# Optimization experiments

Measured on AMD Instinct MI355X. Metric: run time of the kernel, lower is better.

## Reference

```python
import jax, jax.numpy as jnp
import numpy as np

NUM_USER = 60000
NUM_ITEM = 40000
DIM = 64
E_U, E_I, E_G = 720000, 480000, 1200000


def _spmm(vals, src, dst, emb, n_rows):
    # sparse.mm(A, emb): out[dst] += A[dst, src] * emb[src]
    return jax.ops.segment_sum(vals[:, None] * emb[src], dst, num_segments=n_rows)


def setup_inputs() -> dict:
    key = jax.random.key(0)
    ks = jax.random.split(key, 11)
    return {
        "users_emb": jax.random.normal(ks[0], (NUM_USER, DIM), dtype=jnp.float32),
        "items_emb": jax.random.normal(ks[1], (NUM_ITEM, DIM), dtype=jnp.float32),
        "user_src": jax.random.randint(ks[2], (E_U,), 0, NUM_USER, dtype=jnp.int32),
        "user_dst": jax.random.randint(ks[3], (E_U,), 0, NUM_USER, dtype=jnp.int32),
        "user_vals": jax.random.uniform(ks[4], (E_U,), dtype=jnp.float32),
        "item_src": jax.random.randint(ks[5], (E_I,), 0, NUM_ITEM, dtype=jnp.int32),
        "item_dst": jax.random.randint(ks[6], (E_I,), 0, NUM_ITEM, dtype=jnp.int32),
        "item_vals": jax.random.uniform(ks[7], (E_I,), dtype=jnp.float32),
        "graph_src": jax.random.randint(ks[8], (E_G,), 0, NUM_USER + NUM_ITEM, dtype=jnp.int32),
        "graph_dst": jax.random.randint(ks[9], (E_G,), 0, NUM_USER + NUM_ITEM, dtype=jnp.int32),
        "graph_vals": jax.random.uniform(ks[10], (E_G,), dtype=jnp.float32),
    }


def reference(users_emb, items_emb, user_src, user_dst, user_vals,
              item_src, item_dst, item_vals, graph_src, graph_dst, graph_vals):
    num_user, num_item = users_emb.shape[0], items_emb.shape[0]
    # h_u1 = sparse.mm(user_mat, users_emb); h_i1 = sparse.mm(item_mat, items_emb)
    h_u1 = _spmm(user_vals, user_src, user_dst, users_emb, num_user)
    h_i1 = _spmm(item_vals, item_src, item_dst, items_emb, num_item)
    # all_emb_tran = sparse.mm(graph, cat([users_emb, items_emb]))  (unused for mode=0)
    all_emb = jnp.concatenate([users_emb, items_emb], axis=0)
    all_tran = _spmm(graph_vals, graph_src, graph_dst, all_emb, num_user + num_item)
    h_u2, h_i2 = all_tran[:num_user], all_tran[num_user:]
    # mode == 0 -> return (h_u1, h_i1)
    return (h_u1, h_i1)
```

## Files before the change

### kernel.cpp

```cpp
#include <hip/hip_runtime.h>
#include <hip/hip_fp16.h>

#define DIM   64
#define TILE  64
#define TSH   6
#define CHUNK 4096
#define ACHUNK 1024
#define ATHREADS 256
#define CAPMARGIN 256

__global__ void __launch_bounds__(256) spmm_edge_kernel(
    const float* __restrict__ vals, const int* __restrict__ src,
    const int* __restrict__ dst, const float* __restrict__ emb,
    float* __restrict__ out, int n_edges)
{
    int e    = blockIdx.x * 4 + (threadIdx.x >> 6);
    int lane = threadIdx.x & 63;
    if (e >= n_edges) return;
    atomicAdd(&out[(size_t)dst[e] * DIM + lane],
              vals[e] * emb[(size_t)src[e] * DIM + lane]);
}

__global__ void __launch_bounds__(1024) scatter_kernel(
    const int* __restrict__ src_u, const int* __restrict__ dst_u,
    const float* __restrict__ val_u, int n_u, int nblk_u,
    const int* __restrict__ src_i, const int* __restrict__ dst_i,
    const float* __restrict__ val_i, int n_i,
    int nbu, int cap_u, int cap_i,
    int* __restrict__ bcur, int2* __restrict__ pay,
    int nblk_edges, int nblk_cvt,
    const float4* __restrict__ cvt_u, const float4* __restrict__ cvt_i,
    __half2* __restrict__ cvt_dst, long n4u, long n4tot)
{
    __shared__ int  lcnt[1024];
    __shared__ int  lscan[1024];
    __shared__ int  gbase[1024];
    __shared__ int  wsum[16];
    __shared__ int2 stage[CHUNK];
    __shared__ int  gidx[CHUNK];

    if ((int)blockIdx.x >= nblk_edges) {
        int cb = blockIdx.x - nblk_edges;
        int t  = threadIdx.x;
        for (long i = (long)cb * 1024 + t; i < n4tot; i += (long)nblk_cvt * 1024) {
            float4 f = (i < n4u) ? cvt_u[i] : cvt_i[i - n4u];
            cvt_dst[2 * i]     = __floats2half2_rn(f.x, f.y);
            cvt_dst[2 * i + 1] = __floats2half2_rn(f.z, f.w);
        }
        return;
    }

    const int* src; const int* dst; const float* vals;
    int n, bucket_base, base, cap, region_base;
    if ((int)blockIdx.x < nblk_u) {
        src = src_u; dst = dst_u; vals = val_u; n = n_u;
        bucket_base = 0;   base = blockIdx.x * CHUNK;
        cap = cap_u; region_base = 0;
    } else {
        src = src_i; dst = dst_i; vals = val_i; n = n_i;
        bucket_base = nbu; base = (blockIdx.x - nblk_u) * CHUNK;
        cap = cap_i; region_base = nbu * cap_u;
    }

    int tid  = threadIdx.x;
    int wid  = tid >> 6;
    int lane = tid & 63;

    lcnt[tid] = 0;
    __syncthreads();

    int pk[4], vb[4], bk[4], tk[4];
    bool ok[4];
#pragma unroll
    for (int k = 0; k < 4; ++k) {
        int i = base + k * 1024 + tid;
        ok[k] = (i < n);
        if (ok[k]) {
            int s = src[i], d = dst[i];
            vb[k] = __float_as_int(vals[i]);
            bk[k] = d >> TSH;
            pk[k] = (s << TSH) | (d & (TILE - 1));
            tk[k] = atomicAdd(&lcnt[bk[k]], 1);
        }
    }
    __syncthreads();

    int c = lcnt[tid];
    int s = c;
#pragma unroll
    for (int d = 1; d < 64; d <<= 1) {
        int u = __shfl_up(s, d, 64);
        if (lane >= d) s += u;
    }
    if (lane == 63) wsum[wid] = s;
    __syncthreads();
    if (wid == 0 && lane < 16) {
        int v  = wsum[lane];
        int t3 = v;
#pragma unroll
        for (int d = 1; d < 16; d <<= 1) {
            int u = __shfl_up(t3, d, 64);
            if (lane >= d) t3 += u;
        }
        wsum[lane] = t3 - v;
    }
    __syncthreads();
    lscan[tid] = s + wsum[wid];
    gbase[tid] = c ? (region_base + tid * cap +
                      atomicAdd(&bcur[bucket_base + tid], c))
                   : 0;
    __syncthreads();

#pragma unroll
    for (int k = 0; k < 4; ++k) {
        if (ok[k]) {
            int b  = bk[k];
            int sp = lscan[b] - lcnt[b] + tk[k];
            stage[sp] = make_int2(pk[k], vb[k]);
            gidx[sp]  = gbase[b] + tk[k];
        }
    }
    __syncthreads();

    int tot = lscan[1023];
    for (int i = tid; i < tot; i += 1024)
        pay[gidx[i]] = stage[i];
}

struct H4 { __half2 a, b; };

__device__ __forceinline__ float4 gld4(const __half* e, int rowelem, int gl) {
    H4 h = *((const H4*)(e + rowelem) + gl);
    float2 fa = __half22float2(h.a), fb = __half22float2(h.b);
    return make_float4(fa.x, fa.y, fb.x, fb.y);
}
__device__ __forceinline__ float4 gld4(const float* e, int rowelem, int gl) {
    return *((const float4*)(e + rowelem) + gl);
}

template <typename ET>
__global__ void __launch_bounds__(ATHREADS) accum_kernel(
    const int2* __restrict__ pay, const int* __restrict__ bcur, int nbu,
    int cap_u, int cap_i,
    const ET* __restrict__ emb_u, const ET* __restrict__ emb_i,
    float* __restrict__ out_u, float* __restrict__ out_i, int nu, int ni)
{
    __shared__ int2 stage[ACHUNK];
    __shared__ int  rs[TILE];
    __shared__ int  rc[TILE];

    int b = blockIdx.x;
    const ET* emb; float* out; int row0, nrows, start;
    if (b < nbu) {
        emb = emb_u; out = out_u; row0 = b << TSH; nrows = nu;
        start = b * cap_u;
    } else {
        emb = emb_i; out = out_i; row0 = (b - nbu) << TSH; nrows = ni;
        start = nbu * cap_u + (b - nbu) * cap_i;
    }
    int end = start + bcur[b];

    int tid  = threadIdx.x;
    int wid  = tid >> 6;
    int lane = tid & 63;
    int g    = lane >> 4;
    int gl   = lane & 15;
    int grp  = wid * 4 + g;

    float4 acc[4];
#pragma unroll
    for (int k = 0; k < 4; ++k) acc[k] = make_float4(0.f, 0.f, 0.f, 0.f);

    for (int cb = start; cb < end; cb += ACHUNK) {
        int cn = end - cb; if (cn > ACHUNK) cn = ACHUNK;

        if (tid < TILE) rc[tid] = 0;
        __syncthreads();

        int2 e[4]; int rl[4], tk[4]; bool ok[4];
#pragma unroll
        for (int k = 0; k < 4; ++k) {
            int i = tid + ATHREADS * k;
            ok[k] = (i < cn);
            if (ok[k]) {
                e[k]  = pay[cb + i];
                rl[k] = e[k].x & (TILE - 1);
                tk[k] = atomicAdd(&rc[rl[k]], 1);
            }
        }
        __syncthreads();

        if (wid == 0) {
            int c = rc[lane];
            int s = c;
#pragma unroll
            for (int d = 1; d < 64; d <<= 1) {
                int t = __shfl_up(s, d, 64);
                if (lane >= d) s += t;
            }
            rs[lane] = s - c;
        }
        __syncthreads();

#pragma unroll
        for (int k = 0; k < 4; ++k)
            if (ok[k]) stage[rs[rl[k]] + tk[k]] = e[k];
        __syncthreads();

#pragma unroll
        for (int rr = 0; rr < 4; ++rr) {
            int r    = grp * 4 + rr;
            int j    = rs[r];
            int jend = j + rc[r];
            float4 a = acc[rr];
            for (; j + 3 < jend; j += 4) {
                int2 p0 = stage[j], p1 = stage[j + 1], p2 = stage[j + 2], p3 = stage[j + 3];
                float4 g0 = gld4(emb, p0.x & ~(TILE - 1), gl);
                float4 g1 = gld4(emb, p1.x & ~(TILE - 1), gl);
                float4 g2 = gld4(emb, p2.x & ~(TILE - 1), gl);
                float4 g3 = gld4(emb, p3.x & ~(TILE - 1), gl);
                float v0 = __int_as_float(p0.y), v1 = __int_as_float(p1.y);
                float v2 = __int_as_float(p2.y), v3 = __int_as_float(p3.y);
                a.x += v0 * g0.x; a.y += v0 * g0.y; a.z += v0 * g0.z; a.w += v0 * g0.w;
                a.x += v1 * g1.x; a.y += v1 * g1.y; a.z += v1 * g1.z; a.w += v1 * g1.w;
                a.x += v2 * g2.x; a.y += v2 * g2.y; a.z += v2 * g2.z; a.w += v2 * g2.w;
                a.x += v3 * g3.x; a.y += v3 * g3.y; a.z += v3 * g3.z; a.w += v3 * g3.w;
            }
            for (; j < jend; ++j) {
                int2 p = stage[j];
                float4 gg = gld4(emb, p.x & ~(TILE - 1), gl);
                float v = __int_as_float(p.y);
                a.x += v * gg.x; a.y += v * gg.y; a.z += v * gg.z; a.w += v * gg.w;
            }
            acc[rr] = a;
        }
        __syncthreads();
    }

#pragma unroll
    for (int rr = 0; rr < 4; ++rr) {
        int r = row0 + grp * 4 + rr;
        if (r < nrows)
            *((float4*)(out + (size_t)r * DIM) + gl) = acc[rr];
    }
}

extern "C" void kernel_launch(void* const* d_in, const int* in_sizes, int n_in,
                              void* d_out, int out_size, void* d_ws, size_t ws_size,
                              hipStream_t stream)
{
    const float* users_emb = (const float*)d_in[0];
    const float* items_emb = (const float*)d_in[1];
    const int*   user_src  = (const int*)  d_in[2];
    const int*   user_dst  = (const int*)  d_in[3];
    const float* user_vals = (const float*)d_in[4];
    const int*   item_src  = (const int*)  d_in[5];
    const int*   item_dst  = (const int*)  d_in[6];
    const float* item_vals = (const float*)d_in[7];

    const int E_u = in_sizes[2];
    const int E_i = in_sizes[5];
    const int NU  = in_sizes[0] / DIM;
    const int NI  = in_sizes[1] / DIM;

    float* out = (float*)d_out;

    const int NBU = (NU + TILE - 1) / TILE;
    const int NBI = (NI + TILE - 1) / TILE;
    const int NB  = NBU + NBI;

    const int cap_u = (E_u + NBU - 1) / NBU + CAPMARGIN;
    const int cap_i = (E_i + NBI - 1) / NBI + CAPMARGIN;

    size_t hdr_ints    = ((size_t)NB + 1) & ~(size_t)1;
    size_t pay_entries = (size_t)NBU * cap_u + (size_t)NBI * cap_i;
    size_t need_core   = hdr_ints * sizeof(int) + pay_entries * sizeof(int2);
    size_t emb_bytes   = (size_t)(NU + NI) * DIM * sizeof(__half);
    size_t need16      = need_core + emb_bytes;

    if (ws_size < need_core || NU > 65536 || NI > 65536) {
        hipMemsetAsync(d_out, 0, (size_t)out_size * sizeof(float), stream);
        spmm_edge_kernel<<<dim3((E_u + 3) / 4), dim3(256), 0, stream>>>(
            user_vals, user_src, user_dst, users_emb, out, E_u);
        spmm_edge_kernel<<<dim3((E_i + 3) / 4), dim3(256), 0, stream>>>(
            item_vals, item_src, item_dst, items_emb, out + (size_t)NU * DIM, E_i);
        return;
    }

    int*  bcur = (int*)d_ws;
    int2* pay  = (int2*)((int*)d_ws + hdr_ints);

    const bool use_fp16 = (ws_size >= need16);
    __half* embh = (__half*)((char*)d_ws + need_core);

    hipMemsetAsync(bcur, 0, (size_t)NB * sizeof(int), stream);

    const int nblk_u   = (E_u + CHUNK - 1) / CHUNK;
    const int nblk_i   = (E_i + CHUNK - 1) / CHUNK;
    const int nbe      = nblk_u + nblk_i;
    const int nblk_cvt = use_fp16 ? 160 : 0;
    const long n4u     = (long)NU * (DIM / 4);
    const long n4tot   = (long)(NU + NI) * (DIM / 4);

    scatter_kernel<<<dim3(nbe + nblk_cvt), dim3(1024), 0, stream>>>(
        user_src, user_dst, user_vals, E_u, nblk_u,
        item_src, item_dst, item_vals, E_i,
        NBU, cap_u, cap_i, bcur, pay,
        nbe, nblk_cvt,
        (const float4*)users_emb, (const float4*)items_emb,
        (__half2*)embh, n4u, n4tot);

    if (use_fp16) {
        accum_kernel<__half><<<dim3(NB), dim3(ATHREADS), 0, stream>>>(
            pay, bcur, NBU, cap_u, cap_i, embh, embh + (size_t)NU * DIM,
            out, out + (size_t)NU * DIM, NU, NI);
    } else {
        accum_kernel<float><<<dim3(NB), dim3(ATHREADS), 0, stream>>>(
            pay, bcur, NBU, cap_u, cap_i, users_emb, items_emb,
            out, out + (size_t)NU * DIM, NU, NI);
    }
}
```

Measured before the change: 71.50 us.

## Split work into three phases overlapping item scatter with user accumulation

The scatter and accumulate stages are reorganised into three kernels. Phase 1 scatters user edges and converts user embeddings to fp16. Phase 2 scatters item edges and converts item embeddings while also accumulating user rows. Phase 3 accumulates item rows. Accumulation now uses 1024-thread blocks with one row per 16-lane group instead of four rows per group, which raises parallelism per block. The aim is to overlap independent stages and reduce tail idle time, at the cost of an extra kernel launch and a large shared-memory union in phase 2 that may limit occupancy.

```diff
diff --git a/kernel.cpp b/kernel.cpp
--- a/kernel.cpp
+++ b/kernel.cpp
@@ -6,7 +6,6 @@
 #define TSH   6
 #define CHUNK 4096
 #define ACHUNK 1024
-#define ATHREADS 256
 #define CAPMARGIN 256
 
 __global__ void __launch_bounds__(256) spmm_edge_kernel(
@@ -21,56 +20,29 @@
               vals[e] * emb[(size_t)src[e] * DIM + lane]);
 }
 
-__global__ void __launch_bounds__(1024) scatter_kernel(
-    const int* __restrict__ src_u, const int* __restrict__ dst_u,
-    const float* __restrict__ val_u, int n_u, int nblk_u,
-    const int* __restrict__ src_i, const int* __restrict__ dst_i,
-    const float* __restrict__ val_i, int n_i,
-    int nbu, int cap_u, int cap_i,
-    int* __restrict__ bcur, int2* __restrict__ pay,
-    int nblk_edges, int nblk_cvt,
-    const float4* __restrict__ cvt_u, const float4* __restrict__ cvt_i,
-    __half2* __restrict__ cvt_dst, long n4u, long n4tot)
-{
-    __shared__ int  lcnt[1024];
-    __shared__ int  lscan[1024];
-    __shared__ int  gbase[1024];
-    __shared__ int  wsum[16];
-    __shared__ int2 stage[CHUNK];
-    __shared__ int  gidx[CHUNK];
-
-    if ((int)blockIdx.x >= nblk_edges) {
-        int cb = blockIdx.x - nblk_edges;
-        int t  = threadIdx.x;
-        for (long i = (long)cb * 1024 + t; i < n4tot; i += (long)nblk_cvt * 1024) {
-            float4 f = (i < n4u) ? cvt_u[i] : cvt_i[i - n4u];
-            cvt_dst[2 * i]     = __floats2half2_rn(f.x, f.y);
-            cvt_dst[2 * i + 1] = __floats2half2_rn(f.z, f.w);
-        }
-        return;
-    }
-
-    const int* src; const int* dst; const float* vals;
-    int n, bucket_base, base, cap, region_base;
-    if ((int)blockIdx.x < nblk_u) {
-        src = src_u; dst = dst_u; vals = val_u; n = n_u;
-        bucket_base = 0;   base = blockIdx.x * CHUNK;
-        cap = cap_u; region_base = 0;
-    } else {
-        src = src_i; dst = dst_i; vals = val_i; n = n_i;
-        bucket_base = nbu; base = (blockIdx.x - nblk_u) * CHUNK;
-        cap = cap_i; region_base = nbu * cap_u;
-    }
-
-    int tid  = threadIdx.x;
-    int wid  = tid >> 6;
-    int lane = tid & 63;
-
-    lcnt[tid] = 0;
-    __syncthreads();
-
-    int pk[4], vb[4], bk[4], tk[4];
-    bool ok[4];
+struct ScatterSM {
+    int  lcnt[1024], lscan[1024], gbase[1024], wsum[16];
+    int2 stage[CHUNK];
+    int  gidx[CHUNK];
+};
+struct AccumSM {
+    int2 stage[ACHUNK];
+    int  rs[TILE], rc[TILE];
+};
+union SMemBig { ScatterSM s; AccumSM a; };
+
+__device__ __forceinline__ void dev_scatter(
+    ScatterSM& sm,
+    const int* __restrict__ src, const int* __restrict__ dst,
+    const float* __restrict__ vals, int n, int base,
+    int bucket_base, int cap, int region_base,
+    int* __restrict__ bcur, int2* __restrict__ pay)
+{
+    int tid = threadIdx.x, wid = tid >> 6, lane = tid & 63;
+    sm.lcnt[tid] = 0;
+    __syncthreads();
+
+    int pk[4], vb[4], bk[4], tk[4]; bool ok[4];
 #pragma unroll
     for (int k = 0; k < 4; ++k) {
         int i = base + k * 1024 + tid;
@@ -80,55 +52,62 @@
             vb[k] = __float_as_int(vals[i]);
             bk[k] = d >> TSH;
             pk[k] = (s << TSH) | (d & (TILE - 1));
-            tk[k] = atomicAdd(&lcnt[bk[k]], 1);
-        }
-    }
-    __syncthreads();
-
-    int c = lcnt[tid];
-    int s = c;
+            tk[k] = atomicAdd(&sm.lcnt[bk[k]], 1);
+        }
+    }
+    __syncthreads();
+
+    int c = sm.lcnt[tid], s = c;
 #pragma unroll
     for (int d = 1; d < 64; d <<= 1) {
         int u = __shfl_up(s, d, 64);
         if (lane >= d) s += u;
     }
-    if (lane == 63) wsum[wid] = s;
+    if (lane == 63) sm.wsum[wid] = s;
     __syncthreads();
     if (wid == 0 && lane < 16) {
-        int v  = wsum[lane];
-        int t3 = v;
+        int v = sm.wsum[lane], t3 = v;
 #pragma unroll
         for (int d = 1; d < 16; d <<= 1) {
             int u = __shfl_up(t3, d, 64);
             if (lane >= d) t3 += u;
         }
-        wsum[lane] = t3 - v;
-    }
-    __syncthreads();
-    lscan[tid] = s + wsum[wid];
-    gbase[tid] = c ? (region_base + tid * cap +
-                      atomicAdd(&bcur[bucket_base + tid], c))
-                   : 0;
-    __syncthreads();
-
-#pragma unroll
-    for (int k = 0; k < 4; ++k) {
+        sm.wsum[lane] = t3 - v;
+    }
+    __syncthreads();
+    sm.lscan[tid] = s + sm.wsum[wid];
+    sm.gbase[tid] = c ? (region_base + tid * cap +
+                         atomicAdd(&bcur[bucket_base + tid], c)) : 0;
+    __syncthreads();
+
+#pragma unroll
+    for (int k = 0; k < 4; ++k)
         if (ok[k]) {
             int b  = bk[k];
-            int sp = lscan[b] - lcnt[b] + tk[k];
-            stage[sp] = make_int2(pk[k], vb[k]);
-            gidx[sp]  = gbase[b] + tk[k];
-        }
-    }
-    __syncthreads();
-
-    int tot = lscan[1023];
+            int sp = sm.lscan[b] - sm.lcnt[b] + tk[k];
+            sm.stage[sp] = make_int2(pk[k], vb[k]);
+            sm.gidx[sp]  = sm.gbase[b] + tk[k];
+        }
+    __syncthreads();
+
+    int tot = sm.lscan[1023];
     for (int i = tid; i < tot; i += 1024)
-        pay[gidx[i]] = stage[i];
+        pay[sm.gidx[i]] = sm.stage[i];
+}
+
+__device__ __forceinline__ void dev_cvt(
+    const float4* __restrict__ in, __half2* __restrict__ dst,
+    long n4, int rank, int nblk)
+{
+    int t = threadIdx.x;
+    for (long i = (long)rank * 1024 + t; i < n4; i += (long)nblk * 1024) {
+        float4 f = in[i];
+        dst[2 * i]     = __floats2half2_rn(f.x, f.y);
+        dst[2 * i + 1] = __floats2half2_rn(f.z, f.w);
+    }
 }
 
 struct H4 { __half2 a, b; };
-
 __device__ __forceinline__ float4 gld4(const __half* e, int rowelem, int gl) {
     H4 h = *((const H4*)(e + rowelem) + gl);
     float2 fa = __half22float2(h.a), fb = __half22float2(h.b);
@@ -139,110 +118,125 @@
 }
 
 template <typename ET>
-__global__ void __launch_bounds__(ATHREADS) accum_kernel(
-    const int2* __restrict__ pay, const int* __restrict__ bcur, int nbu,
-    int cap_u, int cap_i,
-    const ET* __restrict__ emb_u, const ET* __restrict__ emb_i,
-    float* __restrict__ out_u, float* __restrict__ out_i, int nu, int ni)
-{
-    __shared__ int2 stage[ACHUNK];
-    __shared__ int  rs[TILE];
-    __shared__ int  rc[TILE];
-
-    int b = blockIdx.x;
-    const ET* emb; float* out; int row0, nrows, start;
-    if (b < nbu) {
-        emb = emb_u; out = out_u; row0 = b << TSH; nrows = nu;
-        start = b * cap_u;
-    } else {
-        emb = emb_i; out = out_i; row0 = (b - nbu) << TSH; nrows = ni;
-        start = nbu * cap_u + (b - nbu) * cap_i;
-    }
-    int end = start + bcur[b];
-
+__device__ __forceinline__ void dev_accum(
+    AccumSM& sm, const int2* __restrict__ pay, int cnt, int start,
+    const ET* __restrict__ emb, float* __restrict__ out, int row0, int nrows)
+{
     int tid  = threadIdx.x;
     int wid  = tid >> 6;
     int lane = tid & 63;
-    int g    = lane >> 4;
-    int gl   = lane & 15;
+    int g    = lane >> 4, gl = lane & 15;
     int grp  = wid * 4 + g;
 
-    float4 acc[4];
-#pragma unroll
-    for (int k = 0; k < 4; ++k) acc[k] = make_float4(0.f, 0.f, 0.f, 0.f);
+    float4 a = make_float4(0.f, 0.f, 0.f, 0.f);
+    int end = start + cnt;
 
     for (int cb = start; cb < end; cb += ACHUNK) {
         int cn = end - cb; if (cn > ACHUNK) cn = ACHUNK;
 
-        if (tid < TILE) rc[tid] = 0;
-        __syncthreads();
-
-        int2 e[4]; int rl[4], tk[4]; bool ok[4];
-#pragma unroll
-        for (int k = 0; k < 4; ++k) {
-            int i = tid + ATHREADS * k;
-            ok[k] = (i < cn);
-            if (ok[k]) {
-                e[k]  = pay[cb + i];
-                rl[k] = e[k].x & (TILE - 1);
-                tk[k] = atomicAdd(&rc[rl[k]], 1);
-            }
+        if (tid < TILE) sm.rc[tid] = 0;
+        __syncthreads();
+
+        int2 e; int rl = 0, tk = 0; bool ok = (tid < cn);
+        if (ok) {
+            e  = pay[cb + tid];
+            rl = e.x & (TILE - 1);
+            tk = atomicAdd(&sm.rc[rl], 1);
         }
         __syncthreads();
 
         if (wid == 0) {
-            int c = rc[lane];
-            int s = c;
+            int c = sm.rc[lane], s = c;
 #pragma unroll
             for (int d = 1; d < 64; d <<= 1) {
                 int t = __shfl_up(s, d, 64);
                 if (lane >= d) s += t;
             }
-            rs[lane] = s - c;
-        }
-        __syncthreads();
-
-#pragma unroll
-        for (int k = 0; k < 4; ++k)
-            if (ok[k]) stage[rs[rl[k]] + tk[k]] = e[k];
-        __syncthreads();
-
-#pragma unroll
-        for (int rr = 0; rr < 4; ++rr) {
-            int r    = grp * 4 + rr;
-            int j    = rs[r];
-            int jend = j + rc[r];
-            float4 a = acc[rr];
-            for (; j + 3 < jend; j += 4) {
-                int2 p0 = stage[j], p1 = stage[j + 1], p2 = stage[j + 2], p3 = stage[j + 3];
-                float4 g0 = gld4(emb, p0.x & ~(TILE - 1), gl);
-                float4 g1 = gld4(emb, p1.x & ~(TILE - 1), gl);
-                float4 g2 = gld4(emb, p2.x & ~(TILE - 1), gl);
-                float4 g3 = gld4(emb, p3.x & ~(TILE - 1), gl);
-                float v0 = __int_as_float(p0.y), v1 = __int_as_float(p1.y);
-                float v2 = __int_as_float(p2.y), v3 = __int_as_float(p3.y);
-                a.x += v0 * g0.x; a.y += v0 * g0.y; a.z += v0 * g0.z; a.w += v0 * g0.w;
-                a.x += v1 * g1.x; a.y += v1 * g1.y; a.z += v1 * g1.z; a.w += v1 * g1.w;
-                a.x += v2 * g2.x; a.y += v2 * g2.y; a.z += v2 * g2.z; a.w += v2 * g2.w;
-                a.x += v3 * g3.x; a.y += v3 * g3.y; a.z += v3 * g3.z; a.w += v3 * g3.w;
-            }
-            for (; j < jend; ++j) {
-                int2 p = stage[j];
-                float4 gg = gld4(emb, p.x & ~(TILE - 1), gl);
-                float v = __int_as_float(p.y);
-                a.x += v * gg.x; a.y += v * gg.y; a.z += v * gg.z; a.w += v * gg.w;
-            }
-            acc[rr] = a;
-        }
-        __syncthreads();
-    }
-
-#pragma unroll
-    for (int rr = 0; rr < 4; ++rr) {
-        int r = row0 + grp * 4 + rr;
-        if (r < nrows)
-            *((float4*)(out + (size_t)r * DIM) + gl) = acc[rr];
-    }
+            sm.rs[lane] = s - c;
+        }
+        __syncthreads();
+
+        if (ok) sm.stage[sm.rs[rl] + tk] = e;
+        __syncthreads();
+
+        int j = sm.rs[grp], jend = j + sm.rc[grp];
+        for (; j + 3 < jend; j += 4) {
+            int2 p0 = sm.stage[j], p1 = sm.stage[j + 1],
+                 p2 = sm.stage[j + 2], p3 = sm.stage[j + 3];
+            float4 g0 = gld4(emb, p0.x & ~(TILE - 1), gl);
+            float4 g1 = gld4(emb, p1.x & ~(TILE - 1), gl);
+            float4 g2 = gld4(emb, p2.x & ~(TILE - 1), gl);
+            float4 g3 = gld4(emb, p3.x & ~(TILE - 1), gl);
+            float v0 = __int_as_float(p0.y), v1 = __int_as_float(p1.y);
+            float v2 = __int_as_float(p2.y), v3 = __int_as_float(p3.y);
+            a.x += v0 * g0.x; a.y += v0 * g0.y; a.z += v0 * g0.z; a.w += v0 * g0.w;
+            a.x += v1 * g1.x; a.y += v1 * g1.y; a.z += v1 * g1.z; a.w += v1 * g1.w;
+            a.x += v2 * g2.x; a.y += v2 * g2.y; a.z += v2 * g2.z; a.w += v2 * g2.w;
+            a.x += v3 * g3.x; a.y += v3 * g3.y; a.z += v3 * g3.z; a.w += v3 * g3.w;
+        }
+        for (; j < jend; ++j) {
+            int2 p = sm.stage[j];
+            float4 gg = gld4(emb, p.x & ~(TILE - 1), gl);
+            float v = __int_as_float(p.y);
+            a.x += v * gg.x; a.y += v * gg.y; a.z += v * gg.z; a.w += v * gg.w;
+        }
+        __syncthreads();
+    }
+
+    int r = row0 + grp;
+    if (r < nrows)
+        *((float4*)(out + (size_t)r * DIM) + gl) = a;
+}
+
+__global__ void __launch_bounds__(1024) phase1_kernel(
+    const int* __restrict__ src_u, const int* __restrict__ dst_u,
+    const float* __restrict__ val_u, int n_u, int nblk_u,
+    int cap_u, int* __restrict__ bcur, int2* __restrict__ pay,
+    const float4* __restrict__ cvt_in, __half2* __restrict__ cvt_dst,
+    long n4, int nblk_cvt)
+{
+    __shared__ SMemBig sm;
+    if ((int)blockIdx.x < nblk_u)
+        dev_scatter(sm.s, src_u, dst_u, val_u, n_u, blockIdx.x * CHUNK,
+                    0, cap_u, 0, bcur, pay);
+    else
+        dev_cvt(cvt_in, cvt_dst, n4, blockIdx.x - nblk_u, nblk_cvt);
+}
+
+template <typename ET>
+__global__ void __launch_bounds__(1024) phase2_kernel(
+    const int* __restrict__ src_i, const int* __restrict__ dst_i,
+    const float* __restrict__ val_i, int n_i, int nblk_i,
+    int nbu, int cap_u, int cap_i,
+    int* __restrict__ bcur, int2* __restrict__ pay,
+    const float4* __restrict__ cvt_in, __half2* __restrict__ cvt_dst,
+    long n4, int nblk_cvt,
+    const ET* __restrict__ emb_u, float* __restrict__ out_u, int nu)
+{
+    __shared__ SMemBig sm;
+    int bx = blockIdx.x;
+    if (bx < nblk_i) {
+        dev_scatter(sm.s, src_i, dst_i, val_i, n_i, bx * CHUNK,
+                    nbu, cap_i, nbu * cap_u, bcur, pay);
+    } else if (bx < nblk_i + nblk_cvt) {
+        dev_cvt(cvt_in, cvt_dst, n4, bx - nblk_i, nblk_cvt);
+    } else {
+        int b = bx - nblk_i - nblk_cvt;
+        dev_accum<ET>(sm.a, pay, bcur[b], b * cap_u,
+                      emb_u, out_u, b << TSH, nu);
+    }
+}
+
+template <typename ET>
+__global__ void __launch_bounds__(1024) phase3_kernel(
+    const int2* __restrict__ pay, const int* __restrict__ bcur,
+    int nbu, int cap_u, int cap_i,
+    const ET* __restrict__ emb_i, float* __restrict__ out_i, int ni)
+{
+    __shared__ AccumSM sm;
+    int b = blockIdx.x;
+    dev_accum<ET>(sm, pay, bcur[nbu + b], nbu * cap_u + b * cap_i,
+                  emb_i, out_i, b << TSH, ni);
 }
 
 extern "C" void kernel_launch(void* const* d_in, const int* in_sizes, int n_in,
@@ -295,28 +289,35 @@
 
     hipMemsetAsync(bcur, 0, (size_t)NB * sizeof(int), stream);
 
-    const int nblk_u   = (E_u + CHUNK - 1) / CHUNK;
-    const int nblk_i   = (E_i + CHUNK - 1) / CHUNK;
-    const int nbe      = nblk_u + nblk_i;
-    const int nblk_cvt = use_fp16 ? 160 : 0;
-    const long n4u     = (long)NU * (DIM / 4);
-    const long n4tot   = (long)(NU + NI) * (DIM / 4);
-
-    scatter_kernel<<<dim3(nbe + nblk_cvt), dim3(1024), 0, stream>>>(
+    const int nblk_u  = (E_u + CHUNK - 1) / CHUNK;
+    const int nblk_i  = (E_i + CHUNK - 1) / CHUNK;
+    const int cvt_u_b = use_fp16 ? 128 : 0;
+    const int cvt_i_b = use_fp16 ? 96  : 0;
+    const long n4u    = (long)NU * (DIM / 4);
+    const long n4i    = (long)NI * (DIM / 4);
+
+    phase1_kernel<<<dim3(nblk_u + cvt_u_b), dim3(1024), 0, stream>>>(
         user_src, user_dst, user_vals, E_u, nblk_u,
-        item_src, item_dst, item_vals, E_i,
-        NBU, cap_u, cap_i, bcur, pay,
-        nbe, nblk_cvt,
-        (const float4*)users_emb, (const float4*)items_emb,
-        (__half2*)embh, n4u, n4tot);
+        cap_u, bcur, pay,
+        (const float4*)users_emb, (__half2*)embh, n4u, cvt_u_b);
 
     if (use_fp16) {
-        accum_kernel<__half><<<dim3(NB), dim3(ATHREADS), 0, stream>>>(
-            pay, bcur, NBU, cap_u, cap_i, embh, embh + (size_t)NU * DIM,
-            out, out + (size_t)NU * DIM, NU, NI);
+        phase2_kernel<__half><<<dim3(nblk_i + cvt_i_b + NBU), dim3(1024), 0, stream>>>(
+            item_src, item_dst, item_vals, E_i, nblk_i,
+            NBU, cap_u, cap_i, bcur, pay,
+            (const float4*)items_emb, (__half2*)(embh + (size_t)NU * DIM), n4i, cvt_i_b,
+            embh, out, NU);
+        phase3_kernel<__half><<<dim3(NBI), dim3(1024), 0, stream>>>(
+            pay, bcur, NBU, cap_u, cap_i,
+            embh + (size_t)NU * DIM, out + (size_t)NU * DIM, NI);
     } else {
-        accum_kernel<float><<<dim3(NB), dim3(ATHREADS), 0, stream>>>(
-            pay, bcur, NBU, cap_u, cap_i, users_emb, items_emb,
-            out, out + (size_t)NU * DIM, NU, NI);
-    }
-}
+        phase2_kernel<float><<<dim3(nblk_i + NBU), dim3(1024), 0, stream>>>(
+            item_src, item_dst, item_vals, E_i, nblk_i,
+            NBU, cap_u, cap_i, bcur, pay,
+            (const float4*)items_emb, (__half2*)nullptr, 0, 0,
+            users_emb, out, NU);
+        phase3_kernel<float><<<dim3(NBI), dim3(1024), 0, stream>>>(
+            pay, bcur, NBU, cap_u, cap_i,
+            items_emb, out + (size_t)NU * DIM, NI);
+    }
+}
```

Result: faster. 65.56 us (-8.3%).
